# Kernel optimization log

Hardware: AMD Instinct MI355X
Metric: run time of the kernel (lower is better)

The kernel has to match this reference:

```python
import jax, jax.numpy as jnp
import numpy as np
from jax import lax

V, E, H, K, PAD = 30000, 128, 256, 32, 0
B, T = 128, 256


def setup_inputs() -> dict:
    key = jax.random.key(0)
    ks = jax.random.split(key, 16)

    def n(k, shape, s=0.1):
        return jax.random.normal(k, shape, jnp.float32) * s

    embed = n(ks[0], (V, E)).at[PAD].set(0.0)  # padding_idx row zeroed
    wih_f = n(ks[1], (4 * H, E)); whh_f = n(ks[2], (4 * H, H))
    bih_f = n(ks[3], (4 * H,));   bhh_f = n(ks[4], (4 * H,))
    wih_b = n(ks[5], (4 * H, E)); whh_b = n(ks[6], (4 * H, H))
    bih_b = n(ks[7], (4 * H,));   bhh_b = n(ks[8], (4 * H,))
    w_lin = n(ks[9], (K, 2 * H)); b_lin = n(ks[10], (K,))
    start_t = n(ks[11], (K,)); end_t = n(ks[12], (K,)); trans = n(ks[13], (K, K))
    tokens = jax.random.randint(ks[14], (B, T), 0, V)
    lengths = jax.random.randint(ks[15], (B,), 1, T + 1)
    mask = jnp.arange(T)[None, :] < lengths[:, None]  # mask[:,0] always True
    return {"input": tokens, "mask": mask, "embed": embed,
            "wih_f": wih_f, "whh_f": whh_f, "bih_f": bih_f, "bhh_f": bhh_f,
            "wih_b": wih_b, "whh_b": whh_b, "bih_b": bih_b, "bhh_b": bhh_b,
            "w_lin": w_lin, "b_lin": b_lin,
            "start_t": start_t, "end_t": end_t, "trans": trans}


def _lstm(x, wih, whh, bih, bhh, reverse):
    # x: [B,T,E]; torch gate order i,f,g,o
    Bq, _, _ = x.shape
    Hh = whh.shape[1]
    pre = jnp.einsum('bte,ge->btg', x, wih) + bih + bhh  # [B,T,4H]
    pre = jnp.swapaxes(pre, 0, 1)  # [T,B,4H]

    def step(carry, p):
        h, c = carry
        g = p + h @ whh.T
        i, f, gg, o = jnp.split(g, 4, axis=-1)
        c = jax.nn.sigmoid(f) * c + jax.nn.sigmoid(i) * jnp.tanh(gg)
        h = jax.nn.sigmoid(o) * jnp.tanh(c)
        return (h, c), h

    init = (jnp.zeros((Bq, Hh), x.dtype), jnp.zeros((Bq, Hh), x.dtype))
    _, hs = lax.scan(step, init, pre, reverse=reverse)
    return jnp.swapaxes(hs, 0, 1)  # [B,T,H]


def _emissions(input, embed, wih_f, whh_f, bih_f, bhh_f, wih_b, whh_b, bih_b, bhh_b, w_lin, b_lin):
    x = embed[input]                               # [B,T,E]
    hf = _lstm(x, wih_f, whh_f, bih_f, bhh_f, False)
    hb = _lstm(x, wih_b, whh_b, bih_b, bhh_b, True)
    return jnp.concatenate([hf, hb], -1) @ w_lin.T + b_lin  # [B,T,K]


def _viterbi(em, mask, start_t, end_t, trans):
    Bq, Tq, Kq = em.shape
    score = start_t + em[:, 0]                     # [B,K]
    em_t = jnp.swapaxes(em, 0, 1)[1:]              # [T-1,B,K]
    m_t = jnp.swapaxes(mask, 0, 1)[1:]             # [T-1,B]

    def step(score, em_m):
        emt, m = em_m
        cand = score[:, :, None] + trans[None] + emt[:, None, :]  # [B,K,K]
        best = cand.max(axis=1)
        idx = jnp.argmax(cand, axis=1)             # [B,K] best prev tag
        return jnp.where(m[:, None], best, score), idx

    score, hist = lax.scan(step, score, (em_t, m_t))  # hist [T-1,B,K]
    last = jnp.argmax(score + end_t, axis=-1)      # [B] tag at last valid pos

    def back(idx, hist_m):
        h, m = hist_m
        prev = jnp.take_along_axis(h, idx[:, None], axis=1)[:, 0]
        new = jnp.where(m, prev, idx)
        return new, new

    _, tags_head = lax.scan(back, last, (hist, m_t), reverse=True)  # [T-1,B]
    tags = jnp.concatenate([tags_head, last[None]], axis=0)         # [T,B]
    tags = jnp.swapaxes(tags, 0, 1)
    return jnp.where(mask, tags, 0).astype(jnp.int32)


def reference(input, mask, embed, wih_f, whh_f, bih_f, bhh_f, wih_b, whh_b, bih_b, bhh_b, w_lin, b_lin, start_t, end_t, trans):
    em = _emissions(input, embed, wih_f, whh_f, bih_f, bhh_f,
                    wih_b, whh_b, bih_b, bhh_b, w_lin, b_lin)
    return _viterbi(em, mask, start_t, end_t, trans)
```

## Files before the change

### kernel.cpp

```cpp
#include <hip/hip_runtime.h>
#include <hip/hip_bf16.h>

#define B_ 128
#define T_ 256
#define E_ 128
#define H_ 256
#define K_ 32
#define G4H 1024

__device__ __forceinline__ float sigf(float z) { return 1.0f / (1.0f + expf(-z)); }

__global__ void k_lengths(const unsigned* __restrict__ maskw, int* __restrict__ lengths) {
  __shared__ int flagBad;
  __shared__ int flagOdd;
  int tid = threadIdx.x;
  if (tid == 0) { flagBad = 0; flagOdd = 0; }
  __syncthreads();
  int bad = 0, odd = 0;
  for (int i = tid; i < (B_ * T_) / 4; i += 256) {
    unsigned v = maskw[i];
    if (v > 1u) bad = 1;
    if ((i & 1) && v) odd = 1;
  }
  if (bad) atomicOr(&flagBad, 1);
  if (odd) atomicOr(&flagOdd, 1);
  __syncthreads();
  int mode = flagBad ? 0 : (flagOdd ? 1 : 2);
  for (int b = tid; b < B_; b += 256) {
    int cnt = 0;
    if (mode == 0) {
      const unsigned char* mb = (const unsigned char*)maskw;
      for (int t = 0; t < T_; ++t) cnt += (mb[b * T_ + t] != 0);
    } else if (mode == 1) {
      for (int t = 0; t < T_; ++t) cnt += (maskw[b * T_ + t] != 0);
    } else {
      for (int t = 0; t < T_; ++t) cnt += (maskw[(size_t)(b * T_ + t) * 2] != 0);
    }
    if (cnt < 1) cnt = 1;
    lengths[b] = cnt;
  }
}

__global__ void k_packw2(const float* __restrict__ wih_f, const float* __restrict__ whh_f,
                         const float* __restrict__ wih_b, const float* __restrict__ whh_b,
                         float* __restrict__ wpk) {
  int e = blockIdx.x * 256 + threadIdx.x;
  if (e >= 2 * 8 * 96 * 128 * 4) return;
  int p = e & 3;
  int g = (e >> 2) & 127;
  int rest = e >> 9;
  int k4 = rest % 96;
  int do_ = rest / 96;
  int o = do_ & 7, d = do_ >> 3;
  int ty = g >> 5;
  int brow = ty * 256 + o * 32 + (g & 31);
  int k = k4 * 4 + p;
  const float* wih = d ? wih_b : wih_f;
  const float* whh = d ? whh_b : whh_f;
  float v = (k < E_) ? wih[brow * E_ + k] : whh[brow * H_ + (k - E_)];
  wpk[e] = v;
}

__global__ void k_bias(const float* __restrict__ bih_f, const float* __restrict__ bhh_f,
                       const float* __restrict__ bih_b, const float* __restrict__ bhh_b,
                       float* __restrict__ bias) {
  int e = blockIdx.x * 256 + threadIdx.x;
  if (e >= 2 * G4H) return;
  int d = e >> 10, j = e & 1023;
  bias[e] = d ? (bih_b[j] + bhh_b[j]) : (bih_f[j] + bhh_f[j]);
}

__global__ void k_gather(const int* __restrict__ tokens, const float* __restrict__ embed,
                         float* __restrict__ x) {
  int idx = blockIdx.x * 256 + threadIdx.x;
  int p = idx >> 5, e4 = idx & 31;
  int tok = tokens[p];
  ((float4*)x)[(size_t)p * 32 + e4] = ((const float4*)embed)[(size_t)tok * 32 + e4];
}

__global__ void k_zero(int* __restrict__ flags) {
  int i = blockIdx.x * 256 + threadIdx.x;
  if (i < 256 * 64) flags[i] = 0;
}

__global__ __launch_bounds__(512) void k_lstm2(const float* __restrict__ x,
    const float* __restrict__ wpk, const float* __restrict__ bias,
    float* __restrict__ hf, float* __restrict__ hb,
    float* __restrict__ hx, int* __restrict__ flags) {
  const int wg = blockIdx.x;
  const int o  = wg & 7;
  const int rb = (wg >> 3) & 15;
  const int d  = wg >> 7;
  const int b0 = rb * 8;
  const int tid = threadIdx.x;
  __shared__ float vs[384 * 10];
  __shared__ float gbuf[128 * 10];
  const float4* __restrict__ w4 = (const float4*)(wpk + (size_t)(d * 8 + o) * 96 * 128 * 4);
  const int g = tid & 127, rp = tid >> 7;
  const int ty = g >> 5;
  const int brow = ty * 256 + o * 32 + (g & 31);
  const float bj = bias[d * G4H + brow];
  float* __restrict__ hout = d ? hb : hf;
  float* __restrict__ hxg = hx + (size_t)(d * 16 + rb) * 2 * 2048;
  int* __restrict__ flagg = flags + (d * 16 + rb) * 8 * 64;
  const int uu = (tid & 255) >> 3, rr = tid & 7;
  float creg = 0.f;
  for (int s = 0; s < T_; ++s) {
    const int t = d ? (T_ - 1 - s) : s;
    if (s > 0 && tid < 8) {
      int* fp = flagg + tid * 64;
      while (__hip_atomic_load(fp, __ATOMIC_RELAXED, __HIP_MEMORY_SCOPE_AGENT) < s) {}
    }
    __syncthreads();
    {
      int idx = tid;
#pragma unroll
      for (int j = 0; j < 2; ++j, idx += 512) {
        int r = idx >> 7, e = idx & 127;
        vs[e * 10 + r] = x[((size_t)(b0 + r) * T_ + t) * E_ + e];
      }
    }
    if (s == 0) {
      int idx = tid;
#pragma unroll
      for (int j = 0; j < 4; ++j, idx += 512) {
        int u = idx >> 3, r = idx & 7;
        vs[(E_ + u) * 10 + r] = 0.f;
      }
    } else {
      const float* hsrc = hxg + (size_t)(s & 1) * 2048;
      int idx = tid;
#pragma unroll
      for (int j = 0; j < 4; ++j, idx += 512) {
        int u = idx >> 3, r = idx & 7;
        float hv = __hip_atomic_load((float*)(hsrc + idx), __ATOMIC_RELAXED, __HIP_MEMORY_SCOPE_AGENT);
        vs[(E_ + u) * 10 + r] = hv;
      }
    }
    __syncthreads();
    float a0 = bj, a1 = bj;
    const float* vsp = vs + rp * 2;
#pragma unroll 8
    for (int k4 = 0; k4 < 96; ++k4) {
      float4 w = w4[(size_t)k4 * 128 + g];
      float2 v0 = *(const float2*)(vsp + (4 * k4 + 0) * 10);
      float2 v1 = *(const float2*)(vsp + (4 * k4 + 1) * 10);
      float2 v2 = *(const float2*)(vsp + (4 * k4 + 2) * 10);
      float2 v3 = *(const float2*)(vsp + (4 * k4 + 3) * 10);
      a0 += w.x * v0.x + w.y * v1.x + w.z * v2.x + w.w * v3.x;
      a1 += w.x * v0.y + w.y * v1.y + w.z * v2.y + w.w * v3.y;
    }
    *(float2*)&gbuf[g * 10 + rp * 2] = make_float2(a0, a1);
    __syncthreads();
    if (tid < 256) {
      float ig = gbuf[(uu) * 10 + rr];
      float fg = gbuf[(32 + uu) * 10 + rr];
      float gg = gbuf[(64 + uu) * 10 + rr];
      float og = gbuf[(96 + uu) * 10 + rr];
      creg = sigf(fg) * creg + sigf(ig) * tanhf(gg);
      float hn = sigf(og) * tanhf(creg);
      int ugl = o * 32 + uu;
      hout[((size_t)(b0 + rr) * T_ + t) * H_ + ugl] = hn;
      __hip_atomic_store(hxg + (size_t)((s + 1) & 1) * 2048 + ugl * 8 + rr, hn,
                         __ATOMIC_RELAXED, __HIP_MEMORY_SCOPE_AGENT);
    }
    asm volatile("s_waitcnt vmcnt(0)" ::: "memory");
    __syncthreads();
    if (tid == 0)
      __hip_atomic_store(flagg + o * 64, s + 1, __ATOMIC_RELEASE, __HIP_MEMORY_SCOPE_AGENT);
  }
}

__global__ __launch_bounds__(256) void k_emis(const float* __restrict__ hf, const float* __restrict__ hb,
    const float* __restrict__ w_lin, const float* __restrict__ b_lin, float* __restrict__ em) {
  __shared__ float hsl[8][512];
  __shared__ float red[8][8][K_];
  const int tid = threadIdx.x;
  const int pos0 = blockIdx.x * 8;
  for (int it = 0; it < 4; ++it) {
    int idx = it * 256 + tid;
    int rr = idx >> 7, c4 = idx & 127;
    const float* src = (c4 < 64) ? (hf + ((size_t)(pos0 + rr)) * H_ + (c4 * 4))
                                 : (hb + ((size_t)(pos0 + rr)) * H_ + ((c4 - 64) * 4));
    float4 v = *(const float4*)src;
    *(float4*)&hsl[rr][c4 * 4] = v;
  }
  __syncthreads();
  const int k = tid & 31, jc = tid >> 5;
  float wreg[64];
#pragma unroll
  for (int i4 = 0; i4 < 16; ++i4) {
    float4 w = *(const float4*)(w_lin + (size_t)k * 512 + jc * 64 + i4 * 4);
    wreg[i4 * 4 + 0] = w.x; wreg[i4 * 4 + 1] = w.y; wreg[i4 * 4 + 2] = w.z; wreg[i4 * 4 + 3] = w.w;
  }
  float acc[8];
  for (int rr = 0; rr < 8; ++rr) {
    float a = 0.f;
#pragma unroll
    for (int i4 = 0; i4 < 16; ++i4) {
      float4 h = *(const float4*)&hsl[rr][jc * 64 + i4 * 4];
      a += wreg[i4 * 4 + 0] * h.x + wreg[i4 * 4 + 1] * h.y + wreg[i4 * 4 + 2] * h.z + wreg[i4 * 4 + 3] * h.w;
    }
    acc[rr] = a;
  }
  for (int rr2 = 0; rr2 < 8; ++rr2) red[rr2][jc][k] = acc[rr2];
  __syncthreads();
  {
    int rr = tid >> 5, kk = tid & 31;
    float s = b_lin[kk];
#pragma unroll
    for (int j = 0; j < 8; ++j) s += red[rr][j][kk];
    em[((size_t)(pos0 + rr)) * K_ + kk] = s;
  }
}

__global__ __launch_bounds__(64) void k_viterbi(const float* __restrict__ em,
    const int* __restrict__ lengths, const float* __restrict__ start_t,
    const float* __restrict__ end_t, const float* __restrict__ trans,
    int* __restrict__ out) {
  const int b = blockIdx.x;
  const int lane = threadIdx.x;
  __shared__ unsigned char hist[T_ - 1][K_];
  __shared__ float sl[K_];
  const int len = lengths[b];
  float tc[K_];
  float score = 0.f;
  if (lane < K_) {
#pragma unroll
    for (int i = 0; i < K_; ++i) tc[i] = trans[i * K_ + lane];
    score = start_t[lane] + em[((size_t)b * T_) * K_ + lane];
  }
  for (int t = 1; t < T_; ++t) {
    float emk = 0.f;
    if (lane < K_) {
      emk = em[((size_t)b * T_ + t) * K_ + lane];
      sl[lane] = score;
    }
    __syncthreads();
    if (lane < K_) {
      float best = sl[0] + tc[0]; int bi = 0;
#pragma unroll
      for (int i = 1; i < K_; ++i) {
        float c = sl[i] + tc[i];
        if (c > best) { best = c; bi = i; }
      }
      hist[t - 1][lane] = (unsigned char)bi;
      if (t < len) score = best + emk;
    }
    __syncthreads();
  }
  if (lane < K_) sl[lane] = score + end_t[lane];
  __syncthreads();
  int* outb = out + (size_t)b * T_;
  for (int t = lane; t < T_; t += 64)
    if (t >= len) outb[t] = 0;
  if (lane == 0) {
    float best = sl[0]; int cur = 0;
    for (int k2 = 1; k2 < K_; ++k2)
      if (sl[k2] > best) { best = sl[k2]; cur = k2; }
    outb[len - 1] = cur;
    for (int t = len - 2; t >= 0; --t) { cur = hist[t][cur]; outb[t] = cur; }
  }
}

extern "C" void kernel_launch(void* const* d_in, const int* in_sizes, int n_in,
                              void* d_out, int out_size, void* d_ws, size_t ws_size,
                              hipStream_t stream) {
  const int* tokens   = (const int*)d_in[0];
  const unsigned* maskw = (const unsigned*)d_in[1];
  const float* embed  = (const float*)d_in[2];
  const float* wih_f  = (const float*)d_in[3];
  const float* whh_f  = (const float*)d_in[4];
  const float* bih_f  = (const float*)d_in[5];
  const float* bhh_f  = (const float*)d_in[6];
  const float* wih_b  = (const float*)d_in[7];
  const float* whh_b  = (const float*)d_in[8];
  const float* bih_b  = (const float*)d_in[9];
  const float* bhh_b  = (const float*)d_in[10];
  const float* w_lin  = (const float*)d_in[11];
  const float* b_lin  = (const float*)d_in[12];
  const float* start_t = (const float*)d_in[13];
  const float* end_t  = (const float*)d_in[14];
  const float* trans  = (const float*)d_in[15];
  int* out = (int*)d_out;
  (void)in_sizes; (void)n_in; (void)out_size; (void)ws_size;

  char* ws = (char*)d_ws;
  size_t off = 0;
  auto alloc = [&](size_t bytes) { size_t o = off; off = (off + bytes + 255) & ~(size_t)255; return o; };
  int*   lengths = (int*)(ws + alloc((size_t)B_ * 4));
  float* wpk     = (float*)(ws + alloc((size_t)2 * 8 * 96 * 128 * 4 * 4));
  float* bias    = (float*)(ws + alloc((size_t)2 * G4H * 4));
  float* x       = (float*)(ws + alloc((size_t)B_ * T_ * E_ * 4));
  float* hf      = (float*)(ws + alloc((size_t)B_ * T_ * H_ * 4));
  float* hb      = (float*)(ws + alloc((size_t)B_ * T_ * H_ * 4));
  float* em      = (float*)(ws + alloc((size_t)B_ * T_ * K_ * 4));
  float* hx      = (float*)(ws + alloc((size_t)2 * 16 * 2 * 2048 * 4));
  int*   flags   = (int*)(ws + alloc((size_t)256 * 64 * 4));

  k_lengths<<<dim3(1), dim3(256), 0, stream>>>(maskw, lengths);
  k_packw2<<<dim3((2 * 8 * 96 * 128 * 4 + 255) / 256), dim3(256), 0, stream>>>(wih_f, whh_f, wih_b, whh_b, wpk);
  k_bias<<<dim3(8), dim3(256), 0, stream>>>(bih_f, bhh_f, bih_b, bhh_b, bias);
  k_gather<<<dim3((B_ * T_ * E_ / 4) / 256), dim3(256), 0, stream>>>(tokens, embed, x);
  k_zero<<<dim3(64), dim3(256), 0, stream>>>(flags);
  k_lstm2<<<dim3(256), dim3(512), 0, stream>>>(x, wpk, bias, hf, hb, hx, flags);
  k_emis<<<dim3(B_ * T_ / 8), dim3(256), 0, stream>>>(hf, hb, w_lin, b_lin, em);
  k_viterbi<<<dim3(B_), dim3(64), 0, stream>>>(em, lengths, start_t, end_t, trans, out);
}
```

Before: 3.494 ms.

## Keep LSTM weight slice resident in LDS and repartition workgroups to 16 units × 16 rows

After: 3.180 ms. -9.0%, faster.

```diff
diff --git a/kernel.cpp b/kernel.cpp
--- a/kernel.cpp
+++ b/kernel.cpp
@@ -41,24 +41,22 @@
   }
 }
 
-__global__ void k_packw2(const float* __restrict__ wih_f, const float* __restrict__ whh_f,
+__global__ void k_packw4(const float* __restrict__ wih_f, const float* __restrict__ whh_f,
                          const float* __restrict__ wih_b, const float* __restrict__ whh_b,
                          float* __restrict__ wpk) {
   int e = blockIdx.x * 256 + threadIdx.x;
-  if (e >= 2 * 8 * 96 * 128 * 4) return;
+  if (e >= 786432) return;
   int p = e & 3;
-  int g = (e >> 2) & 127;
-  int rest = e >> 9;
+  int g = (e >> 2) & 63;
+  int rest = e >> 8;
   int k4 = rest % 96;
-  int do_ = rest / 96;
-  int o = do_ & 7, d = do_ >> 3;
-  int ty = g >> 5;
-  int brow = ty * 256 + o * 32 + (g & 31);
+  int dus = rest / 96;
+  int us = dus & 15, d = dus >> 4;
+  int brow = (g >> 4) * 256 + us * 16 + (g & 15);
   int k = k4 * 4 + p;
   const float* wih = d ? wih_b : wih_f;
   const float* whh = d ? whh_b : whh_f;
-  float v = (k < E_) ? wih[brow * E_ + k] : whh[brow * H_ + (k - E_)];
-  wpk[e] = v;
+  wpk[e] = (k < E_) ? wih[brow * E_ + k] : whh[brow * H_ + (k - E_)];
 }
 
 __global__ void k_bias(const float* __restrict__ bih_f, const float* __restrict__ bhh_f,
@@ -80,94 +78,115 @@
 
 __global__ void k_zero(int* __restrict__ flags) {
   int i = blockIdx.x * 256 + threadIdx.x;
-  if (i < 256 * 64) flags[i] = 0;
-}
-
-__global__ __launch_bounds__(512) void k_lstm2(const float* __restrict__ x,
+  if (i < 16384) flags[i] = 0;
+}
+
+__global__ __launch_bounds__(512) void k_lstm4(const float* __restrict__ x,
     const float* __restrict__ wpk, const float* __restrict__ bias,
     float* __restrict__ hf, float* __restrict__ hb,
     float* __restrict__ hx, int* __restrict__ flags) {
   const int wg = blockIdx.x;
-  const int o  = wg & 7;
-  const int rb = (wg >> 3) & 15;
+  const int us = wg & 15;
+  const int rb = (wg >> 4) & 7;
   const int d  = wg >> 7;
-  const int b0 = rb * 8;
+  const int b0 = rb * 16;
   const int tid = threadIdx.x;
-  __shared__ float vs[384 * 10];
-  __shared__ float gbuf[128 * 10];
-  const float4* __restrict__ w4 = (const float4*)(wpk + (size_t)(d * 8 + o) * 96 * 128 * 4);
-  const int g = tid & 127, rp = tid >> 7;
-  const int ty = g >> 5;
-  const int brow = ty * 256 + o * 32 + (g & 31);
-  const float bj = bias[d * G4H + brow];
+  __shared__ float4 wL[96 * 64];
+  __shared__ float4 vL[96 * 16];
+  __shared__ float  gbuf2[2 * 64 * 17];
+
+  {
+    const float4* wsrc = (const float4*)(wpk + (size_t)(d * 16 + us) * 24576);
+    for (int i = tid; i < 6144; i += 512) wL[i] = wsrc[i];
+  }
+  const int r2 = tid & 7;
+  const int gg = (tid >> 3) & 31;
+  const int kc = tid >> 8;
+  const int g0 = 2 * gg, g1 = g0 + 1;
+  const int uu = tid & 15, rr = (tid >> 4) & 15;
+  const int sk4 = tid >> 4, sr = tid & 15;
+  float b_i = 0.f, b_f = 0.f, b_g = 0.f, b_o = 0.f;
+  if (tid < 256) {
+    b_i = bias[d * G4H + 0 * 256 + us * 16 + uu];
+    b_f = bias[d * G4H + 1 * 256 + us * 16 + uu];
+    b_g = bias[d * G4H + 2 * 256 + us * 16 + uu];
+    b_o = bias[d * G4H + 3 * 256 + us * 16 + uu];
+  }
+  float creg = 0.f;
+  float4 xr;
+  {
+    int t0 = d ? (T_ - 1) : 0;
+    xr = *(const float4*)(x + ((size_t)(b0 + sr) * T_ + t0) * E_ + sk4 * 4);
+  }
   float* __restrict__ hout = d ? hb : hf;
-  float* __restrict__ hxg = hx + (size_t)(d * 16 + rb) * 2 * 2048;
-  int* __restrict__ flagg = flags + (d * 16 + rb) * 8 * 64;
-  const int uu = (tid & 255) >> 3, rr = tid & 7;
-  float creg = 0.f;
+  float* __restrict__ hxg = hx + (size_t)(d * 8 + rb) * 8192;
+  int* __restrict__ flagg = flags + (d * 8 + rb) * 1024;
+  __syncthreads();
+
   for (int s = 0; s < T_; ++s) {
     const int t = d ? (T_ - 1 - s) : s;
-    if (s > 0 && tid < 8) {
+    if (s > 0 && tid < 16) {
       int* fp = flagg + tid * 64;
       while (__hip_atomic_load(fp, __ATOMIC_RELAXED, __HIP_MEMORY_SCOPE_AGENT) < s) {}
     }
     __syncthreads();
-    {
-      int idx = tid;
-#pragma unroll
-      for (int j = 0; j < 2; ++j, idx += 512) {
-        int r = idx >> 7, e = idx & 127;
-        vs[e * 10 + r] = x[((size_t)(b0 + r) * T_ + t) * E_ + e];
-      }
-    }
+    vL[sk4 * 16 + sr] = xr;
     if (s == 0) {
-      int idx = tid;
-#pragma unroll
-      for (int j = 0; j < 4; ++j, idx += 512) {
-        int u = idx >> 3, r = idx & 7;
-        vs[(E_ + u) * 10 + r] = 0.f;
+#pragma unroll
+      for (int it = 0; it < 8; ++it) {
+        int i = it * 512 + tid;
+        ((float*)vL)[(32 + (i >> 6)) * 64 + (i & 15) * 4 + ((i >> 4) & 3)] = 0.f;
       }
     } else {
-      const float* hsrc = hxg + (size_t)(s & 1) * 2048;
-      int idx = tid;
-#pragma unroll
-      for (int j = 0; j < 4; ++j, idx += 512) {
-        int u = idx >> 3, r = idx & 7;
-        float hv = __hip_atomic_load((float*)(hsrc + idx), __ATOMIC_RELAXED, __HIP_MEMORY_SCOPE_AGENT);
-        vs[(E_ + u) * 10 + r] = hv;
+      const float* hsrc = hxg + (size_t)(s & 1) * 4096;
+#pragma unroll
+      for (int it = 0; it < 8; ++it) {
+        int i = it * 512 + tid;
+        float hv = __hip_atomic_load(hsrc + i, __ATOMIC_RELAXED, __HIP_MEMORY_SCOPE_AGENT);
+        ((float*)vL)[(32 + (i >> 6)) * 64 + (i & 15) * 4 + ((i >> 4) & 3)] = hv;
       }
     }
     __syncthreads();
-    float a0 = bj, a1 = bj;
-    const float* vsp = vs + rp * 2;
-#pragma unroll 8
-    for (int k4 = 0; k4 < 96; ++k4) {
-      float4 w = w4[(size_t)k4 * 128 + g];
-      float2 v0 = *(const float2*)(vsp + (4 * k4 + 0) * 10);
-      float2 v1 = *(const float2*)(vsp + (4 * k4 + 1) * 10);
-      float2 v2 = *(const float2*)(vsp + (4 * k4 + 2) * 10);
-      float2 v3 = *(const float2*)(vsp + (4 * k4 + 3) * 10);
-      a0 += w.x * v0.x + w.y * v1.x + w.z * v2.x + w.w * v3.x;
-      a1 += w.x * v0.y + w.y * v1.y + w.z * v2.y + w.w * v3.y;
-    }
-    *(float2*)&gbuf[g * 10 + rp * 2] = make_float2(a0, a1);
+    if (s + 1 < T_) {
+      int tn = d ? (T_ - 2 - s) : (s + 1);
+      xr = *(const float4*)(x + ((size_t)(b0 + sr) * T_ + tn) * E_ + sk4 * 4);
+    }
+    float a00 = 0.f, a01 = 0.f, a10 = 0.f, a11 = 0.f;
+    {
+      const float4* wp = wL + kc * 48 * 64;
+      const float4* vp = vL + kc * 48 * 16;
+#pragma unroll 4
+      for (int k4 = 0; k4 < 48; ++k4) {
+        float4 w0 = wp[k4 * 64 + g0];
+        float4 w1 = wp[k4 * 64 + g1];
+        float4 v0 = vp[k4 * 16 + 2 * r2];
+        float4 v1 = vp[k4 * 16 + 2 * r2 + 1];
+        a00 += w0.x * v0.x + w0.y * v0.y + w0.z * v0.z + w0.w * v0.w;
+        a01 += w0.x * v1.x + w0.y * v1.y + w0.z * v1.z + w0.w * v1.w;
+        a10 += w1.x * v0.x + w1.y * v0.y + w1.z * v0.z + w1.w * v0.w;
+        a11 += w1.x * v1.x + w1.y * v1.y + w1.z * v1.z + w1.w * v1.w;
+      }
+    }
+    gbuf2[kc * 1088 + g0 * 17 + 2 * r2]     = a00;
+    gbuf2[kc * 1088 + g0 * 17 + 2 * r2 + 1] = a01;
+    gbuf2[kc * 1088 + g1 * 17 + 2 * r2]     = a10;
+    gbuf2[kc * 1088 + g1 * 17 + 2 * r2 + 1] = a11;
     __syncthreads();
     if (tid < 256) {
-      float ig = gbuf[(uu) * 10 + rr];
-      float fg = gbuf[(32 + uu) * 10 + rr];
-      float gg = gbuf[(64 + uu) * 10 + rr];
-      float og = gbuf[(96 + uu) * 10 + rr];
-      creg = sigf(fg) * creg + sigf(ig) * tanhf(gg);
+      float ig = gbuf2[uu * 17 + rr]        + gbuf2[1088 + uu * 17 + rr]        + b_i;
+      float fg = gbuf2[(16 + uu) * 17 + rr] + gbuf2[1088 + (16 + uu) * 17 + rr] + b_f;
+      float gv = gbuf2[(32 + uu) * 17 + rr] + gbuf2[1088 + (32 + uu) * 17 + rr] + b_g;
+      float og = gbuf2[(48 + uu) * 17 + rr] + gbuf2[1088 + (48 + uu) * 17 + rr] + b_o;
+      creg = sigf(fg) * creg + sigf(ig) * tanhf(gv);
       float hn = sigf(og) * tanhf(creg);
-      int ugl = o * 32 + uu;
-      hout[((size_t)(b0 + rr) * T_ + t) * H_ + ugl] = hn;
-      __hip_atomic_store(hxg + (size_t)((s + 1) & 1) * 2048 + ugl * 8 + rr, hn,
+      hout[((size_t)(b0 + rr) * T_ + t) * H_ + us * 16 + uu] = hn;
+      __hip_atomic_store(hxg + (size_t)((s + 1) & 1) * 4096 + (us * 16 + uu) * 16 + rr, hn,
                          __ATOMIC_RELAXED, __HIP_MEMORY_SCOPE_AGENT);
     }
     asm volatile("s_waitcnt vmcnt(0)" ::: "memory");
     __syncthreads();
     if (tid == 0)
-      __hip_atomic_store(flagg + o * 64, s + 1, __ATOMIC_RELEASE, __HIP_MEMORY_SCOPE_AGENT);
+      __hip_atomic_store(flagg + us * 64, s + 1, __ATOMIC_RELEASE, __HIP_MEMORY_SCOPE_AGENT);
   }
 }
 
@@ -289,21 +308,21 @@
   size_t off = 0;
   auto alloc = [&](size_t bytes) { size_t o = off; off = (off + bytes + 255) & ~(size_t)255; return o; };
   int*   lengths = (int*)(ws + alloc((size_t)B_ * 4));
-  float* wpk     = (float*)(ws + alloc((size_t)2 * 8 * 96 * 128 * 4 * 4));
+  float* wpk     = (float*)(ws + alloc((size_t)786432 * 4));
   float* bias    = (float*)(ws + alloc((size_t)2 * G4H * 4));
   float* x       = (float*)(ws + alloc((size_t)B_ * T_ * E_ * 4));
   float* hf      = (float*)(ws + alloc((size_t)B_ * T_ * H_ * 4));
   float* hb      = (float*)(ws + alloc((size_t)B_ * T_ * H_ * 4));
   float* em      = (float*)(ws + alloc((size_t)B_ * T_ * K_ * 4));
-  float* hx      = (float*)(ws + alloc((size_t)2 * 16 * 2 * 2048 * 4));
-  int*   flags   = (int*)(ws + alloc((size_t)256 * 64 * 4));
+  float* hx      = (float*)(ws + alloc((size_t)16 * 8192 * 4));
+  int*   flags   = (int*)(ws + alloc((size_t)16384 * 4));
 
   k_lengths<<<dim3(1), dim3(256), 0, stream>>>(maskw, lengths);
-  k_packw2<<<dim3((2 * 8 * 96 * 128 * 4 + 255) / 256), dim3(256), 0, stream>>>(wih_f, whh_f, wih_b, whh_b, wpk);
+  k_packw4<<<dim3(3072), dim3(256), 0, stream>>>(wih_f, whh_f, wih_b, whh_b, wpk);
   k_bias<<<dim3(8), dim3(256), 0, stream>>>(bih_f, bhh_f, bih_b, bhh_b, bias);
   k_gather<<<dim3((B_ * T_ * E_ / 4) / 256), dim3(256), 0, stream>>>(tokens, embed, x);
   k_zero<<<dim3(64), dim3(256), 0, stream>>>(flags);
-  k_lstm2<<<dim3(256), dim3(512), 0, stream>>>(x, wpk, bias, hf, hb, hx, flags);
+  k_lstm4<<<dim3(256), dim3(512), 0, stream>>>(x, wpk, bias, hf, hb, hx, flags);
   k_emis<<<dim3(B_ * T_ / 8), dim3(256), 0, stream>>>(hf, hb, w_lin, b_lin, em);
   k_viterbi<<<dim3(B_), dim3(64), 0, stream>>>(em, lengths, start_t, end_t, trans, out);
 }
```
